# Performance work log

Measured on AMD Instinct MI355X. Metric: run time of the kernel, lower is better.

## Reference

```python
import jax, jax.numpy as jnp
import numpy as np

N_HEADS = 16
HEAD_DIM = 128

def _apply_rope(x, cos, sin):
    # x: [B, H, T, D]; cos/sin: [T, D//2]
    B, H, T, D = x.shape
    xp = x.astype(jnp.float32).reshape(B, H, T, D // 2, 2)
    x0, x1 = xp[..., 0], xp[..., 1]
    c = cos[None, None, :T, :]
    s = sin[None, None, :T, :]
    # complex multiply (x0 + i x1) * (c + i s)
    r0 = x0 * c - x1 * s
    r1 = x0 * s + x1 * c
    out = jnp.stack([r0, r1], axis=-1).reshape(B, H, T, D)
    return out.astype(x.dtype)

def setup_inputs() -> dict:
    key = jax.random.key(0)
    ks = jax.random.split(key, 7)
    B, T, C = 2, 2048, 2048
    Dh = C // N_HEADS
    sc = 1.0 / np.sqrt(C)
    x = jax.random.normal(ks[0], (B, T, C), dtype=jnp.float32)
    # rotary frequencies like precompute_freqs_cis
    pos = jnp.arange(T, dtype=jnp.float32)
    inv = 1.0 / (10000.0 ** (jnp.arange(0, Dh, 2, dtype=jnp.float32) / Dh))
    ang = pos[:, None] * inv[None, :]  # [T, Dh//2]
    freqs_cos = jnp.cos(ang)
    freqs_sin = jnp.sin(ang)
    wq = jax.random.normal(ks[1], (C, C), dtype=jnp.float32) * sc
    wk = jax.random.normal(ks[2], (C, C), dtype=jnp.float32) * sc
    wv = jax.random.normal(ks[3], (C, C), dtype=jnp.float32) * sc
    wo = jax.random.normal(ks[4], (C, C), dtype=jnp.float32) * sc
    return {"x": x, "freqs_cos": freqs_cos, "freqs_sin": freqs_sin,
            "wq": wq, "wk": wk, "wv": wv, "wo": wo}

def reference(x, freqs_cos, freqs_sin, wq, wk, wv, wo):
    B, T, C = x.shape
    H, D = N_HEADS, HEAD_DIM
    # nn.Linear applies x @ W.T
    q = (x @ wq.T).reshape(B, T, H, D).transpose(0, 2, 1, 3)
    k = (x @ wk.T).reshape(B, T, H, D).transpose(0, 2, 1, 3)
    v = (x @ wv.T).reshape(B, T, H, D).transpose(0, 2, 1, 3)
    q = _apply_rope(q, freqs_cos, freqs_sin)
    k = _apply_rope(k, freqs_cos, freqs_sin)
    scale = 1.0 / np.sqrt(D)
    attn = jnp.einsum('bhqd,bhkd->bhqk', q, k) * scale  # [B,H,T,T]
    causal = jnp.tril(jnp.ones((T, T), dtype=bool))
    attn = jnp.where(causal[None, None], attn, -jnp.inf)
    attn = jax.nn.softmax(attn, axis=-1)
    out = jnp.einsum('bhqk,bhkd->bhqd', attn, v)
    out = out.transpose(0, 2, 1, 3).reshape(B, T, C)
    return out @ wo.T
```

## Files before the change

### kernel.cpp

```cpp
#include <hip/hip_runtime.h>
#include <hip/hip_bf16.h>
#include <stdint.h>


typedef short bf16x8 __attribute__((ext_vector_type(8)));
typedef float f32x4  __attribute__((ext_vector_type(4)));

static __device__ __forceinline__ short f2bf(float f) {
  unsigned u = __builtin_bit_cast(unsigned, f);
  u = (u + 0x7fffu + ((u >> 16) & 1u)) >> 16;
  return (short)u;
}
static __device__ __forceinline__ short f2bf_fast(float f) {
  unsigned u = __builtin_bit_cast(unsigned, f);
  return (short)((u + 0x8000u) >> 16);
}
static __device__ __forceinline__ float bf2f(short s) {
  unsigned u = ((unsigned)(unsigned short)s) << 16;
  return __builtin_bit_cast(float, u);
}
static __device__ __forceinline__ void gload_lds16(const void* g, void* l) {
  auto gp = (const __attribute__((address_space(1))) void*)(g);
  auto lp = (__attribute__((address_space(3))) void*)(l);
  __builtin_amdgcn_global_load_lds(gp, lp, 16, 0, 0);
}
#define VMCNT(n) asm volatile("s_waitcnt vmcnt(" #n ")" ::: "memory")

__global__ __launch_bounds__(256) void cast8_kernel(const float* __restrict__ in,
                                                    short* __restrict__ out, int n8) {
  int g = blockIdx.x * 256 + threadIdx.x;
  if (g >= n8) return;
  const float4* p = (const float4*)(in + (size_t)g * 8);
  float4 a = p[0], b = p[1];
  bf16x8 o;
  o[0] = f2bf(a.x); o[1] = f2bf(a.y); o[2] = f2bf(a.z); o[3] = f2bf(a.w);
  o[4] = f2bf(b.x); o[5] = f2bf(b.y); o[6] = f2bf(b.z); o[7] = f2bf(b.w);
  *(bf16x8*)(out + (size_t)g * 8) = o;
}

__global__ __launch_bounds__(256) void castw_kernel(const float* __restrict__ w0,
                                                    const float* __restrict__ w1,
                                                    const float* __restrict__ w2,
                                                    const float* __restrict__ w3,
                                                    short* __restrict__ out) {
  int seg = blockIdx.y;
  const float* in = (seg == 0) ? w0 : (seg == 1) ? w1 : (seg == 2) ? w2 : w3;
  short* o = out + (size_t)seg * 4194304;
  int g = blockIdx.x * 256 + threadIdx.x;
  const float4* p = (const float4*)(in + (size_t)g * 8);
  float4 a = p[0], b = p[1];
  bf16x8 v;
  v[0] = f2bf(a.x); v[1] = f2bf(a.y); v[2] = f2bf(a.z); v[3] = f2bf(a.w);
  v[4] = f2bf(b.x); v[5] = f2bf(b.y); v[6] = f2bf(b.z); v[7] = f2bf(b.w);
  *(bf16x8*)(o + (size_t)g * 8) = v;
}

__global__ __launch_bounds__(256) void rope_kernel(short* __restrict__ qk,
                                                   const float* __restrict__ cs,
                                                   const float* __restrict__ sn,
                                                   float scale) {
  int g = blockIdx.x * 256 + threadIdx.x;
  size_t e0 = (size_t)g * 8;
  int d0 = (int)(e0 & 127);
  int t  = (int)((e0 >> 7) & 2047);
  bf16x8 v = *(bf16x8*)(qk + e0);
  float4 c = *(const float4*)(cs + t * 64 + (d0 >> 1));
  float4 s = *(const float4*)(sn + t * 64 + (d0 >> 1));
  float cc[4] = {c.x, c.y, c.z, c.w};
  float ss[4] = {s.x, s.y, s.z, s.w};
  bf16x8 o;
#pragma unroll
  for (int i = 0; i < 4; ++i) {
    float x0 = bf2f(v[2 * i]), x1 = bf2f(v[2 * i + 1]);
    o[2 * i]     = f2bf((x0 * cc[i] - x1 * ss[i]) * scale);
    o[2 * i + 1] = f2bf((x0 * ss[i] + x1 * cc[i]) * scale);
  }
  *(bf16x8*)(qk + e0) = o;
}

__global__ __launch_bounds__(256) void transpose_v(const short* __restrict__ vb,
                                                   short* __restrict__ vt) {
  __shared__ char L[8192] __attribute__((aligned(128)));
  int bx = blockIdx.x;
  int bh = bx >> 6, rest = bx & 63, tt = rest >> 1, td = rest & 1;
  int t0 = tt * 64, d0 = td * 64;
  size_t base = (size_t)bh * (2048 * 128);
#pragma unroll
  for (int it = 0; it < 2; ++it) {
    int c = it * 256 + threadIdx.x;
    int t = c >> 3, dc = c & 7;
    bf16x8 v = *(const bf16x8*)(vb + base + (size_t)(t0 + t) * 128 + d0 + dc * 8);
#pragma unroll
    for (int i = 0; i < 8; ++i) {
      int d = dc * 8 + i;
      int g = (d & 7) ^ ((d >> 3) & 7);
      *(short*)(L + d * 128 + (((t >> 3) ^ g) * 16) + (t & 7) * 2) = v[i];
    }
  }
  __syncthreads();
#pragma unroll
  for (int it = 0; it < 2; ++it) {
    int c = it * 256 + threadIdx.x;
    int dr = c >> 3, tc = c & 7;
    int g = (dr & 7) ^ ((dr >> 3) & 7);
    bf16x8 v = *(const bf16x8*)(L + dr * 128 + ((tc ^ g) * 16));
    *(bf16x8*)(vt + base + (size_t)(d0 + dr) * 2048 + t0 + tc * 8) = v;
  }
}

template <int MODE>
__global__ __launch_bounds__(256) void gemm_bt(const short* __restrict__ A,
                                               const short* __restrict__ W0,
                                               const short* __restrict__ W1,
                                               const short* __restrict__ W2,
                                               short* __restrict__ oq,
                                               short* __restrict__ ok_,
                                               short* __restrict__ ov,
                                               float* __restrict__ of, int NT) {
  __shared__ char lds[16384] __attribute__((aligned(128)));
  int nwg = gridDim.x;
  int bid = blockIdx.x;
  int wg = (bid & 7) * (nwg >> 3) + (bid >> 3);
  int mt = wg / NT, nt = wg % NT;
  const int lane = threadIdx.x & 63;
  const int wid = threadIdx.x >> 6;
  const int wr = wid >> 1, wc = wid & 1;
  const int l15 = lane & 15, l4 = lane >> 4;
  const short* Wp;
  int n0, wsel = 0;
  if (MODE == 0) {
    wsel = nt >> 4;
    Wp = (wsel == 0) ? W0 : ((wsel == 1) ? W1 : W2);
    n0 = (nt & 15) * 128;
  } else {
    Wp = W0;
    n0 = nt * 128;
  }
  const int m0 = mt * 128;
  const f32x4 vzero = {0.f, 0.f, 0.f, 0.f};
  f32x4 acc[4][4];
#pragma unroll
  for (int i = 0; i < 4; ++i)
#pragma unroll
    for (int j = 0; j < 4; ++j) acc[i][j] = vzero;
  const short* Ab = A + (size_t)m0 * 2048;
  const short* Wb = Wp + (size_t)n0 * 2048;
  for (int k0 = 0; k0 < 2048; k0 += 32) {
#pragma unroll
    for (int j = 0; j < 2; ++j) {
      int c = j * 256 + (int)threadIdx.x;
      int row = c >> 2, slot = c & 3;
      int ldsoff = (c - lane) * 16;
      gload_lds16(Ab + (size_t)row * 2048 + k0 + slot * 8, lds + ldsoff);
      gload_lds16(Wb + (size_t)row * 2048 + k0 + slot * 8, lds + 8192 + ldsoff);
    }
    __syncthreads();
    bf16x8 af[4], wf[4];
#pragma unroll
    for (int i = 0; i < 4; ++i) {
      af[i] = *(const bf16x8*)(lds + (wr * 64 + i * 16 + l15) * 64 + l4 * 16);
      wf[i] = *(const bf16x8*)(lds + 8192 + (wc * 64 + i * 16 + l15) * 64 + l4 * 16);
    }
#pragma unroll
    for (int i = 0; i < 4; ++i)
#pragma unroll
      for (int j = 0; j < 4; ++j)
        acc[i][j] = __builtin_amdgcn_mfma_f32_16x16x32_bf16(af[i], wf[j], acc[i][j], 0, 0, 0);
    __syncthreads();
  }
#pragma unroll
  for (int mi = 0; mi < 4; ++mi) {
#pragma unroll
    for (int j = 0; j < 4; ++j) {
      int rr = m0 + wr * 64 + mi * 16 + l4 * 4 + j;
#pragma unroll
      for (int ni = 0; ni < 4; ++ni) {
        int cc = n0 + wc * 64 + ni * 16 + l15;
        float v = acc[mi][ni][j];
        if (MODE == 0) {
          int b = rr >> 11, t = rr & 2047, h = cc >> 7, d = cc & 127;
          short* o = (wsel == 0) ? oq : ((wsel == 1) ? ok_ : ov);
          o[(((size_t)b * 16 + h) * 2048 + t) * 128 + d] = f2bf(v);
        } else {
          of[(size_t)rr * 2048 + cc] = v;
        }
      }
    }
  }
}

__global__ __launch_bounds__(256) void attn_kernel(const short* __restrict__ qb,
                                                   const short* __restrict__ kb,
                                                   const short* __restrict__ vt,
                                                   short* __restrict__ aout) {
  __shared__ char lds[40960] __attribute__((aligned(128)));
  const int tid = threadIdx.x;
  const int lane = tid & 63;
  const int w = tid >> 6;
  const int l15 = lane & 15, l4 = lane >> 4;
  const int bid0 = blockIdx.x;
  const int xcd = bid0 & 7, idx = bid0 >> 3;
  const int bh = xcd * 4 + (idx & 3);
  const int qt = 31 - (idx >> 2);
  const size_t base = (size_t)bh * (2048 * 128);
  char* Pb = lds + 32768 + w * 2048;
  const f32x4 vzero = {0.f, 0.f, 0.f, 0.f};
  const int qbase = qt << 6;

  auto stage = [&](int b, int kt) {
#pragma unroll
    for (int j = 0; j < 4; ++j) {
      int c = j * 256 + tid;
      int row = c >> 4, slot = c & 15;
      gload_lds16(kb + base + (size_t)(kt * 64 + row) * 128 + ((slot ^ (row & 7)) * 8),
                  lds + b * 16384 + (c - lane) * 16);
    }
  };

  const int qrow = qbase + w * 16 + l15;
  bf16x8 aq[4];
#pragma unroll
  for (int ks = 0; ks < 4; ++ks)
    aq[ks] = *(const bf16x8*)(qb + base + (size_t)qrow * 128 + ks * 32 + l4 * 8);
  f32x4 accO[8];
#pragma unroll
  for (int nt = 0; nt < 8; ++nt) accO[nt] = vzero;
  float m_[4], l_[4];
#pragma unroll
  for (int j = 0; j < 4; ++j) { m_[j] = -1e30f; l_[j] = 0.f; }

  stage(0, 0);
  VMCNT(0);
  __builtin_amdgcn_s_barrier();

#pragma unroll 1
  for (int kt = 0; kt <= qt; ++kt) {
    const int cbuf = kt & 1;
    if (kt < qt) stage(cbuf ^ 1, kt + 1);
    const char* Kl = lds + cbuf * 16384;

    f32x4 s[4];
    __builtin_amdgcn_s_setprio(1);
#pragma unroll
    for (int ct = 0; ct < 4; ++ct) {
      s[ct] = vzero;
      int kcol = ct * 16 + l15;
#pragma unroll
      for (int ks = 0; ks < 4; ++ks) {
        bf16x8 bk = *(const bf16x8*)(Kl + kcol * 256 + ((ks * 64 + l4 * 16) ^ ((kcol & 7) << 4)));
        s[ct] = __builtin_amdgcn_mfma_f32_16x16x32_bf16(aq[ks], bk, s[ct], 0, 0, 0);
      }
    }
    __builtin_amdgcn_s_setprio(0);
    if (kt == qt) {
#pragma unroll
      for (int ct = 0; ct < 4; ++ct) {
        int kc = kt * 64 + ct * 16 + l15;
#pragma unroll
        for (int j = 0; j < 4; ++j) {
          int r = qbase + w * 16 + l4 * 4 + j;
          if (kc > r) s[ct][j] = -1e30f;
        }
      }
    }
    float mx4[4];
    float need = 0.f;
#pragma unroll
    for (int j = 0; j < 4; ++j) {
      float mx = fmaxf(fmaxf(s[0][j], s[1][j]), fmaxf(s[2][j], s[3][j]));
      mx = fmaxf(mx, __shfl_xor(mx, 1));
      mx = fmaxf(mx, __shfl_xor(mx, 2));
      mx = fmaxf(mx, __shfl_xor(mx, 4));
      mx = fmaxf(mx, __shfl_xor(mx, 8));
      mx4[j] = mx;
      need = fmaxf(need, mx - m_[j]);
    }
    if (__any(need > 4.0f)) {
#pragma unroll
      for (int j = 0; j < 4; ++j) {
        float mn = fmaxf(m_[j], mx4[j]);
        float resc = __expf(m_[j] - mn);
        m_[j] = mn;
        float rs = 0.f;
#pragma unroll
        for (int ct = 0; ct < 4; ++ct) {
          float e = __expf(s[ct][j] - mn);
          s[ct][j] = e;
          rs += e;
        }
        rs += __shfl_xor(rs, 1);
        rs += __shfl_xor(rs, 2);
        rs += __shfl_xor(rs, 4);
        rs += __shfl_xor(rs, 8);
        l_[j] = l_[j] * resc + rs;
#pragma unroll
        for (int nt = 0; nt < 8; ++nt) accO[nt][j] *= resc;
      }
    } else {
#pragma unroll
      for (int j = 0; j < 4; ++j) {
        float rs = 0.f;
#pragma unroll
        for (int ct = 0; ct < 4; ++ct) {
          float e = __expf(s[ct][j] - m_[j]);
          s[ct][j] = e;
          rs += e;
        }
        rs += __shfl_xor(rs, 1);
        rs += __shfl_xor(rs, 2);
        rs += __shfl_xor(rs, 4);
        rs += __shfl_xor(rs, 8);
        l_[j] += rs;
      }
    }
#pragma unroll
    for (int ct = 0; ct < 4; ++ct)
#pragma unroll
      for (int j = 0; j < 4; ++j) {
        int r = l4 * 4 + j, cc = ct * 16 + l15;
        *(short*)(Pb + r * 128 + ((cc * 2) ^ ((r & 7) << 4))) = f2bf_fast(s[ct][j]);
      }
    __threadfence_block();
    __builtin_amdgcn_s_setprio(1);
#pragma unroll
    for (int ks2 = 0; ks2 < 2; ++ks2) {
      bf16x8 pa = *(const bf16x8*)(Pb + l15 * 128 + ((ks2 * 64 + l4 * 16) ^ ((l15 & 7) << 4)));
#pragma unroll
      for (int nt = 0; nt < 8; ++nt) {
        int d = nt * 16 + l15;
        bf16x8 bv = *(const bf16x8*)(vt + base + (size_t)d * 2048 + kt * 64 + ks2 * 32 + l4 * 8);
        accO[nt] = __builtin_amdgcn_mfma_f32_16x16x32_bf16(pa, bv, accO[nt], 0, 0, 0);
      }
    }
    __builtin_amdgcn_s_setprio(0);
    VMCNT(0);
    __builtin_amdgcn_s_barrier();
  }
  const int b = bh >> 4, h = bh & 15;
#pragma unroll
  for (int j = 0; j < 4; ++j) {
    float inv = 1.0f / l_[j];
    int t = qbase + w * 16 + l4 * 4 + j;
    size_t obase = ((size_t)(b * 2048 + t)) * 2048 + h * 128;
#pragma unroll
    for (int nt = 0; nt < 8; ++nt)
      aout[obase + nt * 16 + l15] = f2bf(accO[nt][j] * inv);
  }
}

extern "C" void kernel_launch(void* const* d_in, const int* in_sizes, int n_in,
                              void* d_out, int out_size, void* d_ws, size_t ws_size,
                              hipStream_t stream) {
  const float* x  = (const float*)d_in[0];
  const float* fc = (const float*)d_in[1];
  const float* fs = (const float*)d_in[2];
  const float* wq = (const float*)d_in[3];
  const float* wk = (const float*)d_in[4];
  const float* wv = (const float*)d_in[5];
  const float* wo = (const float*)d_in[6];

  short* ws  = (short*)d_ws;
  short* xb  = ws;
  short* wqb = ws + 8388608;
  short* wkb = ws + 12582912;
  short* wvb = ws + 16777216;
  short* wob = ws + 20971520;
  short* qb  = ws + 25165824;
  short* kb  = ws + 33554432;
  short* vb  = ws + 41943040;
  short* vt  = xb;
  short* aout = vb;

  cast8_kernel<<<4096, 256, 0, stream>>>(x, xb, 1048576);
  castw_kernel<<<dim3(2048, 4), 256, 0, stream>>>(wq, wk, wv, wo, wqb);
  gemm_bt<0><<<1536, 256, 0, stream>>>(xb, wqb, wkb, wvb, qb, kb, vb, nullptr, 48);
  rope_kernel<<<4096, 256, 0, stream>>>(qb, fc, fs, 0.08838834764831845f);
  rope_kernel<<<4096, 256, 0, stream>>>(kb, fc, fs, 1.0f);
  transpose_v<<<2048, 256, 0, stream>>>(vb, vt);
  attn_kernel<<<1024, 256, 0, stream>>>(qb, kb, vt, aout);
  gemm_bt<1><<<512, 256, 0, stream>>>(aout, wob, nullptr, nullptr,
                                      nullptr, nullptr, nullptr, (float*)d_out, 16);
}
```

Measured before the change: 507.7 us.

## Stage V tiles in LDS and pair causal q-tiles per block for balance

The attention kernel now double-buffers V tiles into LDS alongside K via direct global-to-LDS loads, replacing per-lane strided global reads of transposed V inside the PV MFMA loop. Each block processes two query tiles (p and 31-p), so every block does the same amount of causal work, and the grid is halved to 512 blocks. The threadfence is replaced by an lgkmcnt wait. LDS use grows to 72 KB per block, which lowers occupancy, and each block now runs a serial second pass with a pipeline restart.

```diff
diff --git a/kernel.cpp b/kernel.cpp
--- a/kernel.cpp
+++ b/kernel.cpp
@@ -25,6 +25,7 @@
   __builtin_amdgcn_global_load_lds(gp, lp, 16, 0, 0);
 }
 #define VMCNT(n) asm volatile("s_waitcnt vmcnt(" #n ")" ::: "memory")
+#define LGKMCNT0 asm volatile("s_waitcnt lgkmcnt(0)" ::: "memory")
 
 __global__ __launch_bounds__(256) void cast8_kernel(const float* __restrict__ in,
                                                     short* __restrict__ out, int n8) {
@@ -193,158 +194,170 @@
                                                    const short* __restrict__ kb,
                                                    const short* __restrict__ vt,
                                                    short* __restrict__ aout) {
-  __shared__ char lds[40960] __attribute__((aligned(128)));
+  __shared__ char lds[73728] __attribute__((aligned(128)));
   const int tid = threadIdx.x;
   const int lane = tid & 63;
   const int w = tid >> 6;
   const int l15 = lane & 15, l4 = lane >> 4;
-  const int bid0 = blockIdx.x;
-  const int xcd = bid0 & 7, idx = bid0 >> 3;
-  const int bh = xcd * 4 + (idx & 3);
-  const int qt = 31 - (idx >> 2);
+  int bid0 = blockIdx.x;
+  int bid = (bid0 & 7) * 64 + (bid0 >> 3);
+  const int bh = bid >> 4, p = bid & 15;
   const size_t base = (size_t)bh * (2048 * 128);
-  char* Pb = lds + 32768 + w * 2048;
+  char* Pb = lds + 65536 + w * 2048;
   const f32x4 vzero = {0.f, 0.f, 0.f, 0.f};
-  const int qbase = qt << 6;
 
   auto stage = [&](int b, int kt) {
 #pragma unroll
     for (int j = 0; j < 4; ++j) {
       int c = j * 256 + tid;
-      int row = c >> 4, slot = c & 15;
-      gload_lds16(kb + base + (size_t)(kt * 64 + row) * 128 + ((slot ^ (row & 7)) * 8),
-                  lds + b * 16384 + (c - lane) * 16);
+      int ldsoff = (c - lane) * 16;
+      {
+        int row = c >> 4, slot = c & 15;
+        gload_lds16(kb + base + (size_t)(kt * 64 + row) * 128 + ((slot ^ (row & 7)) * 8),
+                    lds + b * 32768 + ldsoff);
+      }
+      {
+        int row = c >> 3, slot = c & 7;
+        gload_lds16(vt + base + (size_t)row * 2048 + kt * 64 + ((slot ^ (row & 7)) * 8),
+                    lds + b * 32768 + 16384 + ldsoff);
+      }
     }
   };
 
-  const int qrow = qbase + w * 16 + l15;
-  bf16x8 aq[4];
-#pragma unroll
-  for (int ks = 0; ks < 4; ++ks)
-    aq[ks] = *(const bf16x8*)(qb + base + (size_t)qrow * 128 + ks * 32 + l4 * 8);
-  f32x4 accO[8];
-#pragma unroll
-  for (int nt = 0; nt < 8; ++nt) accO[nt] = vzero;
-  float m_[4], l_[4];
-#pragma unroll
-  for (int j = 0; j < 4; ++j) { m_[j] = -1e30f; l_[j] = 0.f; }
-
-  stage(0, 0);
-  VMCNT(0);
-  __builtin_amdgcn_s_barrier();
-
 #pragma unroll 1
-  for (int kt = 0; kt <= qt; ++kt) {
-    const int cbuf = kt & 1;
-    if (kt < qt) stage(cbuf ^ 1, kt + 1);
-    const char* Kl = lds + cbuf * 16384;
-
-    f32x4 s[4];
-    __builtin_amdgcn_s_setprio(1);
-#pragma unroll
-    for (int ct = 0; ct < 4; ++ct) {
-      s[ct] = vzero;
-      int kcol = ct * 16 + l15;
-#pragma unroll
-      for (int ks = 0; ks < 4; ++ks) {
-        bf16x8 bk = *(const bf16x8*)(Kl + kcol * 256 + ((ks * 64 + l4 * 16) ^ ((kcol & 7) << 4)));
-        s[ct] = __builtin_amdgcn_mfma_f32_16x16x32_bf16(aq[ks], bk, s[ct], 0, 0, 0);
-      }
-    }
-    __builtin_amdgcn_s_setprio(0);
-    if (kt == qt) {
-#pragma unroll
-      for (int ct = 0; ct < 4; ++ct) {
-        int kc = kt * 64 + ct * 16 + l15;
-#pragma unroll
-        for (int j = 0; j < 4; ++j) {
-          int r = qbase + w * 16 + l4 * 4 + j;
-          if (kc > r) s[ct][j] = -1e30f;
-        }
-      }
-    }
-    float mx4[4];
-    float need = 0.f;
-#pragma unroll
-    for (int j = 0; j < 4; ++j) {
-      float mx = fmaxf(fmaxf(s[0][j], s[1][j]), fmaxf(s[2][j], s[3][j]));
-      mx = fmaxf(mx, __shfl_xor(mx, 1));
-      mx = fmaxf(mx, __shfl_xor(mx, 2));
-      mx = fmaxf(mx, __shfl_xor(mx, 4));
-      mx = fmaxf(mx, __shfl_xor(mx, 8));
-      mx4[j] = mx;
-      need = fmaxf(need, mx - m_[j]);
-    }
-    if (__any(need > 4.0f)) {
-#pragma unroll
-      for (int j = 0; j < 4; ++j) {
-        float mn = fmaxf(m_[j], mx4[j]);
-        float resc = __expf(m_[j] - mn);
-        m_[j] = mn;
-        float rs = 0.f;
-#pragma unroll
-        for (int ct = 0; ct < 4; ++ct) {
-          float e = __expf(s[ct][j] - mn);
-          s[ct][j] = e;
-          rs += e;
-        }
-        rs += __shfl_xor(rs, 1);
-        rs += __shfl_xor(rs, 2);
-        rs += __shfl_xor(rs, 4);
-        rs += __shfl_xor(rs, 8);
-        l_[j] = l_[j] * resc + rs;
-#pragma unroll
-        for (int nt = 0; nt < 8; ++nt) accO[nt][j] *= resc;
-      }
-    } else {
-#pragma unroll
-      for (int j = 0; j < 4; ++j) {
-        float rs = 0.f;
-#pragma unroll
-        for (int ct = 0; ct < 4; ++ct) {
-          float e = __expf(s[ct][j] - m_[j]);
-          s[ct][j] = e;
-          rs += e;
-        }
-        rs += __shfl_xor(rs, 1);
-        rs += __shfl_xor(rs, 2);
-        rs += __shfl_xor(rs, 4);
-        rs += __shfl_xor(rs, 8);
-        l_[j] += rs;
-      }
-    }
-#pragma unroll
-    for (int ct = 0; ct < 4; ++ct)
-#pragma unroll
-      for (int j = 0; j < 4; ++j) {
-        int r = l4 * 4 + j, cc = ct * 16 + l15;
-        *(short*)(Pb + r * 128 + ((cc * 2) ^ ((r & 7) << 4))) = f2bf_fast(s[ct][j]);
-      }
-    __threadfence_block();
-    __builtin_amdgcn_s_setprio(1);
-#pragma unroll
-    for (int ks2 = 0; ks2 < 2; ++ks2) {
-      bf16x8 pa = *(const bf16x8*)(Pb + l15 * 128 + ((ks2 * 64 + l4 * 16) ^ ((l15 & 7) << 4)));
-#pragma unroll
-      for (int nt = 0; nt < 8; ++nt) {
-        int d = nt * 16 + l15;
-        bf16x8 bv = *(const bf16x8*)(vt + base + (size_t)d * 2048 + kt * 64 + ks2 * 32 + l4 * 8);
-        accO[nt] = __builtin_amdgcn_mfma_f32_16x16x32_bf16(pa, bv, accO[nt], 0, 0, 0);
-      }
-    }
-    __builtin_amdgcn_s_setprio(0);
+  for (int half = 0; half < 2; ++half) {
+    const int qtile = half ? (31 - p) : p;
+    const int qbase = qtile << 6;
+    const int qrow = qbase + w * 16 + l15;
+    bf16x8 aq[4];
+#pragma unroll
+    for (int ks = 0; ks < 4; ++ks)
+      aq[ks] = *(const bf16x8*)(qb + base + (size_t)qrow * 128 + ks * 32 + l4 * 8);
+    f32x4 accO[8];
+#pragma unroll
+    for (int nt = 0; nt < 8; ++nt) accO[nt] = vzero;
+    float m_[4], l_[4];
+#pragma unroll
+    for (int j = 0; j < 4; ++j) { m_[j] = -1e30f; l_[j] = 0.f; }
+
+    stage(0, 0);
     VMCNT(0);
     __builtin_amdgcn_s_barrier();
-  }
-  const int b = bh >> 4, h = bh & 15;
-#pragma unroll
-  for (int j = 0; j < 4; ++j) {
-    float inv = 1.0f / l_[j];
-    int t = qbase + w * 16 + l4 * 4 + j;
-    size_t obase = ((size_t)(b * 2048 + t)) * 2048 + h * 128;
-#pragma unroll
-    for (int nt = 0; nt < 8; ++nt)
-      aout[obase + nt * 16 + l15] = f2bf(accO[nt][j] * inv);
+
+#pragma unroll 1
+    for (int kt = 0; kt <= qtile; ++kt) {
+      const int cbuf = kt & 1;
+      if (kt < qtile) stage(cbuf ^ 1, kt + 1);
+      const char* Kl = lds + cbuf * 32768;
+      const char* Vl = Kl + 16384;
+
+      f32x4 s[4];
+      __builtin_amdgcn_s_setprio(1);
+#pragma unroll
+      for (int ct = 0; ct < 4; ++ct) {
+        s[ct] = vzero;
+        int kcol = ct * 16 + l15;
+#pragma unroll
+        for (int ks = 0; ks < 4; ++ks) {
+          bf16x8 bk = *(const bf16x8*)(Kl + kcol * 256 + ((ks * 64 + l4 * 16) ^ ((kcol & 7) << 4)));
+          s[ct] = __builtin_amdgcn_mfma_f32_16x16x32_bf16(aq[ks], bk, s[ct], 0, 0, 0);
+        }
+      }
+      __builtin_amdgcn_s_setprio(0);
+      if (kt == qtile) {
+#pragma unroll
+        for (int ct = 0; ct < 4; ++ct) {
+          int kc = kt * 64 + ct * 16 + l15;
+#pragma unroll
+          for (int j = 0; j < 4; ++j) {
+            int r = qbase + w * 16 + l4 * 4 + j;
+            if (kc > r) s[ct][j] = -1e30f;
+          }
+        }
+      }
+      float mx4[4];
+      float need = 0.f;
+#pragma unroll
+      for (int j = 0; j < 4; ++j) {
+        float mx = fmaxf(fmaxf(s[0][j], s[1][j]), fmaxf(s[2][j], s[3][j]));
+        mx = fmaxf(mx, __shfl_xor(mx, 1));
+        mx = fmaxf(mx, __shfl_xor(mx, 2));
+        mx = fmaxf(mx, __shfl_xor(mx, 4));
+        mx = fmaxf(mx, __shfl_xor(mx, 8));
+        mx4[j] = mx;
+        need = fmaxf(need, mx - m_[j]);
+      }
+      if (__any(need > 4.0f)) {
+#pragma unroll
+        for (int j = 0; j < 4; ++j) {
+          float mn = fmaxf(m_[j], mx4[j]);
+          float resc = __expf(m_[j] - mn);
+          m_[j] = mn;
+          float rs = 0.f;
+#pragma unroll
+          for (int ct = 0; ct < 4; ++ct) {
+            float e = __expf(s[ct][j] - mn);
+            s[ct][j] = e;
+            rs += e;
+          }
+          rs += __shfl_xor(rs, 1);
+          rs += __shfl_xor(rs, 2);
+          rs += __shfl_xor(rs, 4);
+          rs += __shfl_xor(rs, 8);
+          l_[j] = l_[j] * resc + rs;
+#pragma unroll
+          for (int nt = 0; nt < 8; ++nt) accO[nt][j] *= resc;
+        }
+      } else {
+#pragma unroll
+        for (int j = 0; j < 4; ++j) {
+          float rs = 0.f;
+#pragma unroll
+          for (int ct = 0; ct < 4; ++ct) {
+            float e = __expf(s[ct][j] - m_[j]);
+            s[ct][j] = e;
+            rs += e;
+          }
+          rs += __shfl_xor(rs, 1);
+          rs += __shfl_xor(rs, 2);
+          rs += __shfl_xor(rs, 4);
+          rs += __shfl_xor(rs, 8);
+          l_[j] += rs;
+        }
+      }
+#pragma unroll
+      for (int ct = 0; ct < 4; ++ct)
+#pragma unroll
+        for (int j = 0; j < 4; ++j) {
+          int r = l4 * 4 + j, cc = ct * 16 + l15;
+          *(short*)(Pb + r * 128 + ((cc * 2) ^ ((r & 7) << 4))) = f2bf_fast(s[ct][j]);
+        }
+      LGKMCNT0;
+      __builtin_amdgcn_s_setprio(1);
+#pragma unroll
+      for (int ks2 = 0; ks2 < 2; ++ks2) {
+        bf16x8 pa = *(const bf16x8*)(Pb + l15 * 128 + ((ks2 * 64 + l4 * 16) ^ ((l15 & 7) << 4)));
+#pragma unroll
+        for (int nt = 0; nt < 8; ++nt) {
+          int d = nt * 16 + l15;
+          bf16x8 bv = *(const bf16x8*)(Vl + d * 128 + ((ks2 * 64 + l4 * 16) ^ ((d & 7) << 4)));
+          accO[nt] = __builtin_amdgcn_mfma_f32_16x16x32_bf16(pa, bv, accO[nt], 0, 0, 0);
+        }
+      }
+      __builtin_amdgcn_s_setprio(0);
+      VMCNT(0);
+      __builtin_amdgcn_s_barrier();
+    }
+    const int b = bh >> 4, h = bh & 15;
+#pragma unroll
+    for (int j = 0; j < 4; ++j) {
+      float inv = 1.0f / l_[j];
+      int t = qbase + w * 16 + l4 * 4 + j;
+      size_t obase = ((size_t)(b * 2048 + t)) * 2048 + h * 128;
+#pragma unroll
+      for (int nt = 0; nt < 8; ++nt)
+        aout[obase + nt * 16 + l15] = f2bf(accO[nt][j] * inv);
+    }
   }
 }
 
@@ -377,7 +390,7 @@
   rope_kernel<<<4096, 256, 0, stream>>>(qb, fc, fs, 0.08838834764831845f);
   rope_kernel<<<4096, 256, 0, stream>>>(kb, fc, fs, 1.0f);
   transpose_v<<<2048, 256, 0, stream>>>(vb, vt);
-  attn_kernel<<<1024, 256, 0, stream>>>(qb, kb, vt, aout);
+  attn_kernel<<<512, 256, 0, stream>>>(qb, kb, vt, aout);
   gemm_bt<1><<<512, 256, 0, stream>>>(aout, wob, nullptr, nullptr,
                                       nullptr, nullptr, nullptr, (float*)d_out, 16);
 }
```

Result: faster. 471.3 us (-7.2%).
